# Performance work log

Measured on AMD Instinct MI355X. Metric: run time of the kernel, lower is better.

The kernel has to match this reference:

```python
import jax, jax.numpy as jnp
import numpy as np

L, H, M, KB = 8, 512, 32, 256  # layers, hidden, fourier modes, key bits
EPS = 1e-5


def setup_inputs() -> dict:
    key = jax.random.key(0)
    ks = jax.random.split(key, 20)
    B, S = 8, 2048
    s = 0.02
    return {
        'x': jax.random.normal(ks[0], (B, S), jnp.float32),
        # input projection Linear(1, H): weight [H] (squeezed), bias [H]
        'in_w': jax.random.normal(ks[1], (H,), jnp.float32) * s,
        'in_b': jax.random.normal(ks[2], (H,), jnp.float32) * s,
        # per-layer fourier weights (complex, stored as real/imag), conv1d(k=1), layernorm
        'fw_r': jax.random.normal(ks[3], (L, M, H, H), jnp.float32) * s,
        'fw_i': jax.random.normal(ks[4], (L, M, H, H), jnp.float32) * s,
        'conv_w': jax.random.normal(ks[5], (L, H, H), jnp.float32) / np.sqrt(H),
        'conv_b': jax.random.normal(ks[6], (L, H), jnp.float32) * s,
        'ln_g': jnp.ones((L, H), jnp.float32),
        'ln_b': jnp.zeros((L, H), jnp.float32),
        # output projection H -> H/2 -> H/4 -> 1
        'op1_w': jax.random.normal(ks[7], (H // 2, H), jnp.float32) / np.sqrt(H),
        'op1_b': jnp.zeros((H // 2,), jnp.float32),
        'op2_w': jax.random.normal(ks[8], (H // 4, H // 2), jnp.float32) / np.sqrt(H // 2),
        'op2_b': jnp.zeros((H // 4,), jnp.float32),
        'op3_w': jax.random.normal(ks[9], (1, H // 4), jnp.float32) / np.sqrt(H // 4),
        'op3_b': jnp.zeros((1,), jnp.float32),
        # cryptanalytic head H -> H -> KB (sigmoid)
        'h1_w': jax.random.normal(ks[10], (H, H), jnp.float32) / np.sqrt(H),
        'h1_b': jnp.zeros((H,), jnp.float32),
        'h2_w': jax.random.normal(ks[11], (KB, H), jnp.float32) / np.sqrt(H),
        'h2_b': jnp.zeros((KB,), jnp.float32),
    }


def _gelu(x):
    return jax.nn.gelu(x, approximate=False)


def _fourier_layer(x, Wc, cw, cb, g, b):
    # x: [B, S, H]; Wc: [M, H, H] complex
    S = x.shape[1]
    x_ft = jnp.fft.rfft(x, axis=1)  # [B, F, H] complex, F = S//2+1
    m = min(M, x_ft.shape[1])
    # batched per-mode complex GEMM (replaces python loop over modes)
    spec = jnp.einsum('bmh,mhk->bmk', x_ft[:, :m], Wc[:m])
    out_ft = jnp.concatenate([spec, jnp.zeros_like(x_ft[:, m:])], axis=1)
    x_fourier = jnp.fft.irfft(out_ft, n=S, axis=1)  # real [B, S, H]
    x_conv = x @ cw.T + cb  # Conv1d kernel-size-1 == per-position linear
    y = x_fourier + x_conv
    mu = jnp.mean(y, axis=-1, keepdims=True)
    var = jnp.var(y, axis=-1, keepdims=True)
    return (y - mu) * jax.lax.rsqrt(var + EPS) * g + b


def reference(x, in_w, in_b, fw_r, fw_i, conv_w, conv_b, ln_g, ln_b,
              op1_w, op1_b, op2_w, op2_b, op3_w, op3_b,
              h1_w, h1_b, h2_w, h2_b):
    # input projection: Linear(1, H) on x[..., None]
    h = x[:, :, None] * in_w[None, None, :] + in_b  # [B, S, H]
    Wc = fw_r + 1j * fw_i  # [L, M, H, H]
    for l in range(L):
        h = _fourier_layer(h, Wc[l], conv_w[l], conv_b[l], ln_g[l], ln_b[l]) + h
    # output projection (dropout is identity in eval)
    o = _gelu(h @ op1_w.T + op1_b)
    o = _gelu(o @ op2_w.T + op2_b)
    output = (o @ op3_w.T + op3_b)[..., 0]  # [B, S]
    gf = jnp.mean(h, axis=1)  # [B, H]
    k = _gelu(gf @ h1_w.T + h1_b)
    key_pred = jax.nn.sigmoid(k @ h2_w.T + h2_b)  # [B, KB]
    return output, key_pred
```

## Files before the change

kernel.cpp:

```cpp
#include <hip/hip_runtime.h>
#include <hip/hip_bf16.h>
#include <math.h>

#define BB   8
#define SEQ  2048
#define HD   512
#define LAY  8
#define MD   32
#define NKB  256
#define LNEPS 1e-5f

typedef __attribute__((ext_vector_type(8))) short v8s;
typedef __attribute__((ext_vector_type(4))) float v4f;
typedef __attribute__((ext_vector_type(4))) unsigned short v4us;

__device__ __forceinline__ float b2f(__hip_bfloat16 v) { return __bfloat162float(v); }
__device__ __forceinline__ float geluf(float v) { return v * 0.5f * (1.f + erff(v * 0.70710678118654752f)); }

__device__ __forceinline__ float ldin(const void* p, size_t i, int bf) {
    if (bf) return __bfloat162float(((const __hip_bfloat16*)p)[i]);
    return ((const float*)p)[i];
}
__device__ __forceinline__ void stout(void* p, size_t i, float v, int bf) {
    if (bf) ((__hip_bfloat16*)p)[i] = __float2bfloat16(v);
    else    ((float*)p)[i] = v;
}

__device__ __forceinline__ void gl2lds16(const void* g, void* l) {
    __builtin_amdgcn_global_load_lds((__attribute__((address_space(1))) void*)g,
                                     (__attribute__((address_space(3))) void*)l, 16, 0, 0);
}

__global__ void k_flag(const unsigned int* __restrict__ lng_bits, int* __restrict__ flag) {
    if (threadIdx.x == 0 && blockIdx.x == 0)
        *flag = (lng_bits[0] == 0x3F803F80u) ? 1 : 0;
}

__global__ void k_ffwd(__hip_bfloat16* __restrict__ F) {
    int idx = blockIdx.x * 256 + threadIdx.x;
    int j = idx >> 11, s = idx & 2047;
    int m = j >> 1;
    int phase = (m * s) & (SEQ - 1);
    float ang = (float)phase * (6.283185307179586f / (float)SEQ);
    float v = (j & 1) ? -sinf(ang) : cosf(ang);
    F[idx] = __float2bfloat16(v);
}

__global__ void k_t2(__hip_bfloat16* __restrict__ T2) {
    int idx = blockIdx.x * 256 + threadIdx.x;
    int s = idx >> 6, j = idx & 63;
    int m = j >> 1;
    float v;
    if (j == 0)      v = 1.f / (float)SEQ;
    else if (j == 1) v = 0.f;
    else {
        int phase = (m * s) & (SEQ - 1);
        float ang = (float)phase * (6.283185307179586f / (float)SEQ);
        v = (j & 1) ? (-2.f / (float)SEQ) * sinf(ang) : (2.f / (float)SEQ) * cosf(ang);
    }
    T2[idx] = __float2bfloat16(v);
}

__global__ void k_cwbf(const void* __restrict__ cw, __hip_bfloat16* __restrict__ dst,
                       const int* __restrict__ flag) {
    int bf = *flag;
    int idx = blockIdx.x * 256 + threadIdx.x;
    dst[idx] = __float2bfloat16(ldin(cw, idx, bf));
}

__global__ void k_bfcvt(const void* __restrict__ src, __hip_bfloat16* __restrict__ dst,
                        int n, const int* __restrict__ flag) {
    int bf = *flag;
    int idx = blockIdx.x * 256 + threadIdx.x;
    if (idx < n) dst[idx] = __float2bfloat16(ldin(src, idx, bf));
}

__global__ void k_tr(const void* __restrict__ src, float* __restrict__ dst, int log2R, int C, int n,
                     const int* __restrict__ flag) {
    int bf = *flag;
    int idx = blockIdx.x * 256 + threadIdx.x;
    if (idx >= n) return;
    int R = 1 << log2R;
    int r = idx & (R - 1);
    int c = idx >> log2R;
    dst[idx] = ldin(src, (size_t)r * C + c, bf);
}

__global__ void k_in(const void* __restrict__ x, const void* __restrict__ in_w, const void* __restrict__ in_b,
                     float* __restrict__ h, __hip_bfloat16* __restrict__ hbf, const int* __restrict__ flag) {
    int bf = *flag;
    int idx = blockIdx.x * 256 + threadIdx.x;
    int j = idx & 511;
    int bs = idx >> 9;
    float v = ldin(x, bs, bf) * ldin(in_w, j, bf) + ldin(in_b, j, bf);
    h[idx] = v;
    hbf[idx] = __float2bfloat16(v);
}

__global__ __launch_bounds__(256) void k_fdft2(const __hip_bfloat16* __restrict__ hbf,
                                               const __hip_bfloat16* __restrict__ Ffwd,
                                               float* __restrict__ Xft) {
    __shared__ __align__(16) __hip_bfloat16 Als[16 * 72];
    int t = threadIdx.x;
    int lane = t & 63, wv = t >> 6;
    int ln15 = lane & 15, quad = lane >> 4;
    int ht = blockIdx.x, b = blockIdx.y;
    int sr = t >> 2, hc = (t & 3) * 4;

    v4f acc = (v4f){0.f, 0.f, 0.f, 0.f};

    const __hip_bfloat16* asrc0 = hbf + (size_t)b * SEQ * HD + ht * 16;
    const __hip_bfloat16* fbase = Ffwd + (size_t)(wv * 16 + ln15) * SEQ + quad * 8;

    v4us cur = *(const v4us*)(asrc0 + (size_t)sr * HD + hc);
    for (int kc = 0; kc < 32; kc++) {
#pragma unroll
        for (int e = 0; e < 4; e++)
            Als[(hc + e) * 72 + sr] = ((const __hip_bfloat16*)&cur)[e];
        __syncthreads();
        v4us nxt = cur;
        if (kc < 31)
            nxt = *(const v4us*)(asrc0 + (size_t)((kc + 1) * 64 + sr) * HD + hc);
        v8s bf0 = *(const v8s*)(fbase + kc * 64);
        v8s bf1 = *(const v8s*)(fbase + kc * 64 + 32);
        v8s af0 = *(const v8s*)&Als[ln15 * 72 + quad * 8];
        v8s af1 = *(const v8s*)&Als[ln15 * 72 + 32 + quad * 8];
        acc = __builtin_amdgcn_mfma_f32_16x16x32_bf16(af0, bf0, acc, 0, 0, 0);
        acc = __builtin_amdgcn_mfma_f32_16x16x32_bf16(af1, bf1, acc, 0, 0, 0);
        __syncthreads();
        cur = nxt;
    }
    int j = wv * 16 + ln15;
    int m = j >> 1, c = j & 1;
    int hg = ht * 16 + quad * 4;
#pragma unroll
    for (int r = 0; r < 4; r++)
        Xft[(size_t)(b * 32 + m) * 1024 + (size_t)(hg + r) * 2 + c] = acc[r];
}

__global__ __launch_bounds__(512) void k_mix(const float* __restrict__ Xft,
                                             const void* __restrict__ fwr, const void* __restrict__ fwi,
                                             __hip_bfloat16* __restrict__ spec2, int l,
                                             const int* __restrict__ flag) {
    int bf = *flag;
    int kt = blockIdx.x;
    int m  = blockIdx.y;
    int t = threadIdx.x;
    int kl = t & 31, hg = t >> 5;
    int k0 = kt * 64 + kl * 2;
    __shared__ float xs[8192];
    __shared__ float red[16 * 512];
    for (int e = t; e < 8192; e += 512) {
        int b = e >> 10, r = e & 1023;
        xs[b * 1024 + r] = Xft[(size_t)(b * 32 + m) * 1024 + r];
    }
    __syncthreads();
    float ar0[8], ar1[8], ai0[8], ai1[8];
#pragma unroll
    for (int b = 0; b < 8; b++) { ar0[b] = 0.f; ar1[b] = 0.f; ai0[b] = 0.f; ai1[b] = 0.f; }
    size_t wbase = (size_t)(l * 32 + m) * 262144 + k0;
    const float2* xs2 = (const float2*)xs;
    if (bf) {
        const __hip_bfloat16* fr = (const __hip_bfloat16*)fwr;
        const __hip_bfloat16* fi = (const __hip_bfloat16*)fwi;
        for (int hh = hg; hh < 512; hh += 16) {
            unsigned int ur = *(const unsigned int*)(fr + wbase + (size_t)hh * 512);
            unsigned int ui = *(const unsigned int*)(fi + wbase + (size_t)hh * 512);
            float wr0 = __uint_as_float((ur & 0xFFFFu) << 16);
            float wr1 = __uint_as_float(ur & 0xFFFF0000u);
            float wi0 = __uint_as_float((ui & 0xFFFFu) << 16);
            float wi1 = __uint_as_float(ui & 0xFFFF0000u);
#pragma unroll
            for (int b = 0; b < 8; b++) {
                float2 x2 = xs2[b * 512 + hh];
                ar0[b] += x2.x * wr0 - x2.y * wi0;  ai0[b] += x2.x * wi0 + x2.y * wr0;
                ar1[b] += x2.x * wr1 - x2.y * wi1;  ai1[b] += x2.x * wi1 + x2.y * wr1;
            }
        }
    } else {
        const float* fr = (const float*)fwr;
        const float* fi = (const float*)fwi;
        for (int hh = hg; hh < 512; hh += 16) {
            float2 fr2 = *(const float2*)(fr + wbase + (size_t)hh * 512);
            float2 fi2 = *(const float2*)(fi + wbase + (size_t)hh * 512);
#pragma unroll
            for (int b = 0; b < 8; b++) {
                float2 x2 = xs2[b * 512 + hh];
                ar0[b] += x2.x * fr2.x - x2.y * fi2.x;  ai0[b] += x2.x * fi2.x + x2.y * fr2.x;
                ar1[b] += x2.x * fr2.y - x2.y * fi2.y;  ai1[b] += x2.x * fi2.y + x2.y * fr2.y;
            }
        }
    }
#pragma unroll
    for (int b = 0; b < 8; b++) {
        red[hg * 512 + b * 64 + kl * 2]     = ar0[b];
        red[hg * 512 + b * 64 + kl * 2 + 1] = ar1[b];
    }
    __syncthreads();
    float sr = 0.f;
#pragma unroll
    for (int g = 0; g < 16; g++) sr += red[g * 512 + t];
    __syncthreads();
#pragma unroll
    for (int b = 0; b < 8; b++) {
        red[hg * 512 + b * 64 + kl * 2]     = ai0[b];
        red[hg * 512 + b * 64 + kl * 2 + 1] = ai1[b];
    }
    __syncthreads();
    float si = 0.f;
#pragma unroll
    for (int g = 0; g < 16; g++) si += red[g * 512 + t];

    int b = t >> 6, j = t & 63;
    int k = kt * 64 + j;
    size_t o = ((size_t)(b * 512 + k) << 6) + 2 * m;
    __hip_bfloat16 hr = __float2bfloat16(sr), hi = __float2bfloat16(si);
    unsigned int pk = (unsigned int)*(unsigned short*)&hr | ((unsigned int)*(unsigned short*)&hi << 16);
    *(unsigned int*)(spec2 + o) = pk;
}

__global__ __launch_bounds__(256) void k_gemm(const __hip_bfloat16* __restrict__ hbf,
                                              const __hip_bfloat16* __restrict__ cwbf,
                                              const __hip_bfloat16* __restrict__ T2,
                                              const __hip_bfloat16* __restrict__ spec2,
                                              const void* __restrict__ cb,
                                              __hip_bfloat16* __restrict__ ybf,
                                              int l, const int* __restrict__ flag) {
    int bfv = *flag;
    __shared__ __hip_bfloat16 Als[128 * 32];
    __shared__ __hip_bfloat16 Bls[128 * 32];
    int t = threadIdx.x;
    int lane = t & 63, wv = t >> 6;
    int wr = wv >> 1, wc = wv & 1;
    int ln15 = lane & 15, quad = lane >> 4;
    int row0 = blockIdx.x * 128, n0 = blockIdx.y * 128;
    int b = row0 >> 11;
    int s0 = row0 & 2047;

    v4f acc[16];
#pragma unroll
    for (int i = 0; i < 16; i++) acc[i] = (v4f){0.f, 0.f, 0.f, 0.f};

    const __hip_bfloat16* cwl = cwbf + (size_t)l * 262144;
    for (int kc = 0; kc < 18; kc++) {
        int k0 = kc * 32;
#pragma unroll
        for (int p = 0; p < 2; p++) {
            int i = p * 256 + t;
            int row = i >> 2, kq = (i & 3) * 8;
            const __hip_bfloat16 *asrc, *bsrc;
            if (k0 < 512) {
                asrc = hbf + (size_t)(row0 + row) * 512 + k0 + kq;
                bsrc = cwl + (size_t)(n0 + row) * 512 + k0 + kq;
            } else {
                asrc = T2 + (size_t)(s0 + row) * 64 + (k0 - 512) + kq;
                bsrc = spec2 + (size_t)(b * 512 + n0 + row) * 64 + (k0 - 512) + kq;
            }
            gl2lds16(asrc, &Als[(size_t)(p * 256 + wv * 64) * 8]);
            gl2lds16(bsrc, &Bls[(size_t)(p * 256 + wv * 64) * 8]);
        }
        __syncthreads();
        v8s af[4], bfr[4];
#pragma unroll
        for (int i = 0; i < 4; i++)
            af[i] = *(const v8s*)&Als[(wr * 64 + i * 16 + ln15) * 32 + quad * 8];
#pragma unroll
        for (int j = 0; j < 4; j++)
            bfr[j] = *(const v8s*)&Bls[(wc * 64 + j * 16 + ln15) * 32 + quad * 8];
#pragma unroll
        for (int i = 0; i < 4; i++)
#pragma unroll
            for (int j = 0; j < 4; j++)
                acc[i * 4 + j] = __builtin_amdgcn_mfma_f32_16x16x32_bf16(af[i], bfr[j], acc[i * 4 + j], 0, 0, 0);
        __syncthreads();
    }
#pragma unroll
    for (int j = 0; j < 4; j++) {
        int col = n0 + wc * 64 + j * 16 + ln15;
        float cbv = ldin(cb, l * HD + col, bfv);
#pragma unroll
        for (int i = 0; i < 4; i++) {
            int rg = row0 + wr * 64 + i * 16 + quad * 4;
#pragma unroll
            for (int r = 0; r < 4; r++)
                ybf[(size_t)(rg + r) * HD + col] = __float2bfloat16(acc[i * 4 + j][r] + cbv);
        }
    }
}

__global__ __launch_bounds__(256) void k_ln(const __hip_bfloat16* __restrict__ ybf,
                                            const void* __restrict__ g, const void* __restrict__ bb,
                                            float* __restrict__ h, __hip_bfloat16* __restrict__ hbf,
                                            int l, const int* __restrict__ flag) {
    int bf = *flag;
    int row = blockIdx.x;
    int t = threadIdx.x;
    const unsigned int* yr = (const unsigned int*)(ybf + (size_t)row * HD);
    unsigned int u = yr[t];
    float v0 = __uint_as_float((u & 0xFFFFu) << 16);
    float v1 = __uint_as_float(u & 0xFFFF0000u);
    float s = v0 + v1, q = v0 * v0 + v1 * v1;
#pragma unroll
    for (int o = 32; o > 0; o >>= 1) { s += __shfl_down(s, o); q += __shfl_down(q, o); }
    __shared__ float sm[8];
    __shared__ float mv[2];
    int wid = t >> 6;
    if ((t & 63) == 0) { sm[wid] = s; sm[wid + 4] = q; }
    __syncthreads();
    if (t == 0) {
        float S = sm[0] + sm[1] + sm[2] + sm[3];
        float Q = sm[4] + sm[5] + sm[6] + sm[7];
        float mu = S * (1.f / (float)HD);
        float var = Q * (1.f / (float)HD) - mu * mu;
        mv[0] = mu; mv[1] = rsqrtf(var + LNEPS);
    }
    __syncthreads();
    float mu = mv[0], rs = mv[1];
    float2* hr2 = (float2*)(h + (size_t)row * HD);
    float2 hv = hr2[t];
    float n0 = (v0 - mu) * rs * ldin(g, l * HD + 2 * t, bf)     + ldin(bb, l * HD + 2 * t, bf)     + hv.x;
    float n1 = (v1 - mu) * rs * ldin(g, l * HD + 2 * t + 1, bf) + ldin(bb, l * HD + 2 * t + 1, bf) + hv.y;
    hr2[t] = (float2){n0, n1};
    __hip_bfloat16 a0 = __float2bfloat16(n0), a1 = __float2bfloat16(n1);
    unsigned int up = ((unsigned int)(*(unsigned short*)&a1) << 16) | (unsigned int)(*(unsigned short*)&a0);
    ((unsigned int*)(hbf + (size_t)row * HD))[t] = up;
}

__global__ __launch_bounds__(256) void k_pj1(const __hip_bfloat16* __restrict__ hbf,
                                             const __hip_bfloat16* __restrict__ w1bf,
                                             const void* __restrict__ b1,
                                             __hip_bfloat16* __restrict__ o1bf,
                                             const int* __restrict__ flag) {
    int bfv = *flag;
    __shared__ __hip_bfloat16 Als[128 * 32];
    __shared__ __hip_bfloat16 Bls[128 * 32];
    int t = threadIdx.x;
    int lane = t & 63, wv = t >> 6;
    int wr = wv >> 1, wc = wv & 1;
    int ln15 = lane & 15, quad = lane >> 4;
    int row0 = blockIdx.x * 128, n0 = blockIdx.y * 128;

    v4f acc[16];
#pragma unroll
    for (int i = 0; i < 16; i++) acc[i] = (v4f){0.f, 0.f, 0.f, 0.f};

    for (int kc = 0; kc < 16; kc++) {
        int k0 = kc * 32;
#pragma unroll
        for (int p = 0; p < 2; p++) {
            int i = p * 256 + t;
            int row = i >> 2, kq = (i & 3) * 8;
            gl2lds16(hbf + (size_t)(row0 + row) * 512 + k0 + kq, &Als[(size_t)(p * 256 + wv * 64) * 8]);
            gl2lds16(w1bf + (size_t)(n0 + row) * 512 + k0 + kq, &Bls[(size_t)(p * 256 + wv * 64) * 8]);
        }
        __syncthreads();
        v8s af[4], bfr[4];
#pragma unroll
        for (int i = 0; i < 4; i++)
            af[i] = *(const v8s*)&Als[(wr * 64 + i * 16 + ln15) * 32 + quad * 8];
#pragma unroll
        for (int j = 0; j < 4; j++)
            bfr[j] = *(const v8s*)&Bls[(wc * 64 + j * 16 + ln15) * 32 + quad * 8];
#pragma unroll
        for (int i = 0; i < 4; i++)
#pragma unroll
            for (int j = 0; j < 4; j++)
                acc[i * 4 + j] = __builtin_amdgcn_mfma_f32_16x16x32_bf16(af[i], bfr[j], acc[i * 4 + j], 0, 0, 0);
        __syncthreads();
    }
#pragma unroll
    for (int j = 0; j < 4; j++) {
        int col = n0 + wc * 64 + j * 16 + ln15;
        float bv = ldin(b1, col, bfv);
#pragma unroll
        for (int i = 0; i < 4; i++) {
            int rg = row0 + wr * 64 + i * 16 + quad * 4;
#pragma unroll
            for (int r = 0; r < 4; r++)
                o1bf[(size_t)(rg + r) * 256 + col] = __float2bfloat16(geluf(acc[i * 4 + j][r] + bv));
        }
    }
}

__global__ __launch_bounds__(256) void k_pj2(const __hip_bfloat16* __restrict__ o1bf,
                                             const __hip_bfloat16* __restrict__ w2bf,
                                             const void* __restrict__ b2,
                                             const void* __restrict__ w3, const void* __restrict__ b3,
                                             void* __restrict__ out, const int* __restrict__ flag) {
    int bfv = *flag;
    __shared__ __hip_bfloat16 Als[128 * 32];
    __shared__ __hip_bfloat16 Bls[128 * 32];
    __shared__ __hip_bfloat16 o2s[128 * 130];
    __shared__ float w3s[128];
    int t = threadIdx.x;
    int lane = t & 63, wv = t >> 6;
    int wr = wv >> 1, wc = wv & 1;
    int ln15 = lane & 15, quad = lane >> 4;
    int row0 = blockIdx.x * 128;
    if (t < 128) w3s[t] = ldin(w3, t, bfv);

    v4f acc[16];
#pragma unroll
    for (int i = 0; i < 16; i++) acc[i] = (v4f){0.f, 0.f, 0.f, 0.f};

    for (int kc = 0; kc < 8; kc++) {
        int k0 = kc * 32;
#pragma unroll
        for (int p = 0; p < 2; p++) {
            int i = p * 256 + t;
            int row = i >> 2, kq = (i & 3) * 8;
            gl2lds16(o1bf + (size_t)(row0 + row) * 256 + k0 + kq, &Als[(size_t)(p * 256 + wv * 64) * 8]);
            gl2lds16(w2bf + (size_t)row * 256 + k0 + kq,          &Bls[(size_t)(p * 256 + wv * 64) * 8]);
        }
        __syncthreads();
        v8s af[4], bfr[4];
#pragma unroll
        for (int i = 0; i < 4; i++)
            af[i] = *(const v8s*)&Als[(wr * 64 + i * 16 + ln15) * 32 + quad * 8];
#pragma unroll
        for (int j = 0; j < 4; j++)
            bfr[j] = *(const v8s*)&Bls[(wc * 64 + j * 16 + ln15) * 32 + quad * 8];
#pragma unroll
        for (int i = 0; i < 4; i++)
#pragma unroll
            for (int j = 0; j < 4; j++)
                acc[i * 4 + j] = __builtin_amdgcn_mfma_f32_16x16x32_bf16(af[i], bfr[j], acc[i * 4 + j], 0, 0, 0);
        __syncthreads();
    }
#pragma unroll
    for (int j = 0; j < 4; j++) {
        int col = wc * 64 + j * 16 + ln15;
        float bv = ldin(b2, col, bfv);
#pragma unroll
        for (int i = 0; i < 4; i++) {
            int rl = wr * 64 + i * 16 + quad * 4;
#pragma unroll
            for (int r = 0; r < 4; r++)
                o2s[(rl + r) * 130 + col] = __float2bfloat16(geluf(acc[i * 4 + j][r] + bv));
        }
    }
    __syncthreads();
    if (t < 128) {
        float s = 0.f;
        for (int j = 0; j < 128; j++) s += b2f(o2s[t * 130 + j]) * w3s[j];
        stout(out, row0 + t, s + ldin(b3, 0, bfv), bfv);
    }
}

__global__ void k_zero(float* p, int n) {
    int i = blockIdx.x * 256 + threadIdx.x;
    if (i < n) p[i] = 0.f;
}

__global__ __launch_bounds__(512) void k_gf(const float* __restrict__ h, float* __restrict__ gf) {
    int sc = blockIdx.x, b = blockIdx.y;
    int j = threadIdx.x;
    const float* p = h + ((size_t)b * SEQ + sc * 64) * HD + j;
    float s = 0.f;
    for (int i = 0; i < 64; i++) s += p[(size_t)i * HD];
    atomicAdd(&gf[b * HD + j], s * (1.f / (float)SEQ));
}

__global__ __launch_bounds__(512) void k_head(const float* __restrict__ gf,
                                              const float* __restrict__ h1T, const void* __restrict__ h1b,
                                              const float* __restrict__ h2T, const void* __restrict__ h2b,
                                              void* __restrict__ out, const int* __restrict__ flag) {
    int bf = *flag;
    int b = blockIdx.x;
    int t = threadIdx.x;
    __shared__ float gs[512];
    __shared__ float ks[512];
    gs[t] = gf[b * HD + t];
    __syncthreads();
    float a = 0.f;
    for (int j = 0; j < 512; j++) a += gs[j] * h1T[j * 512 + t];
    ks[t] = geluf(a + ldin(h1b, t, bf));
    __syncthreads();
    if (t < 256) {
        float s = 0.f;
        for (int j = 0; j < 512; j++) s += ks[j] * h2T[j * 256 + t];
        s += ldin(h2b, t, bf);
        stout(out, BB * SEQ + b * NKB + t, 1.f / (1.f + expf(-s)), bf);
    }
}

extern "C" void kernel_launch(void* const* d_in, const int* in_sizes, int n_in,
                              void* d_out, int out_size, void* d_ws, size_t ws_size,
                              hipStream_t stream) {
    const void* x    = d_in[0];
    const void* in_w = d_in[1];
    const void* in_b = d_in[2];
    const void* fwr  = d_in[3];
    const void* fwi  = d_in[4];
    const void* cw   = d_in[5];
    const void* cb   = d_in[6];
    const void* lng  = d_in[7];
    const void* lnb  = d_in[8];
    const void* w1   = d_in[9];
    const void* b1   = d_in[10];
    const void* w2   = d_in[11];
    const void* b2   = d_in[12];
    const void* w3   = d_in[13];
    const void* b3   = d_in[14];
    const void* h1w  = d_in[15];
    const void* h1b  = d_in[16];
    const void* h2w  = d_in[17];
    const void* h2b  = d_in[18];

    float* ws = (float*)d_ws;
    __hip_bfloat16* Ffwd = (__hip_bfloat16*)ws;
    float*          h    = ws + 131072;
    float*          Xp   = h + 8388608;
    __hip_bfloat16* ybf  = (__hip_bfloat16*)Xp;
    __hip_bfloat16* hbf  = (__hip_bfloat16*)(Xp + 4194304);
    __hip_bfloat16* cwbf = (__hip_bfloat16*)(Xp + 8388608);
    __hip_bfloat16* T2   = (__hip_bfloat16*)(Xp + 10485760);
    __hip_bfloat16* spec2= (__hip_bfloat16*)(Xp + 10551296);
    float*          Xft  = Xp + 10682368;
    float*          gf   = Xft + 262144;
    float*          w1T  = gf + 4096;
    __hip_bfloat16* w1bf = (__hip_bfloat16*)w1T;
    __hip_bfloat16* w2bf = (__hip_bfloat16*)(w1T + 65536);
    float*          w2T  = w1T + 131072;
    float*          h1T  = w2T + 32768;
    float*          h2T  = h1T + 262144;
    int*            flag = (int*)(h2T + 131072);
    __hip_bfloat16* o1bf = ybf;

    k_flag<<<1, 1, 0, stream>>>((const unsigned int*)lng, flag);
    k_ffwd<<<512, 256, 0, stream>>>(Ffwd);
    k_t2<<<512, 256, 0, stream>>>(T2);
    k_cwbf<<<8192, 256, 0, stream>>>(cw, cwbf, flag);
    k_bfcvt<<<512, 256, 0, stream>>>(w1, w1bf, 131072, flag);
    k_bfcvt<<<128, 256, 0, stream>>>(w2, w2bf, 32768, flag);
    k_tr<<<1024, 256, 0, stream>>>(h1w, h1T, 9, 512, 262144, flag);
    k_tr<<<512, 256, 0, stream>>>(h2w, h2T, 8, 512, 131072, flag);
    k_in<<<32768, 256, 0, stream>>>(x, in_w, in_b, h, hbf, flag);

    for (int l = 0; l < LAY; l++) {
        k_fdft2<<<dim3(32, 8), 256, 0, stream>>>(hbf, Ffwd, Xft);
        k_mix<<<dim3(8, 32), 512, 0, stream>>>(Xft, fwr, fwi, spec2, l, flag);
        k_gemm<<<dim3(128, 4), 256, 0, stream>>>(hbf, cwbf, T2, spec2, cb, ybf, l, flag);
        k_ln<<<16384, 256, 0, stream>>>(ybf, lng, lnb, h, hbf, l, flag);
    }

    k_zero<<<16, 256, 0, stream>>>(gf, 4096);
    k_gf<<<dim3(32, 8), 512, 0, stream>>>(h, gf);
    k_pj1<<<dim3(128, 2), 256, 0, stream>>>(hbf, w1bf, b1, o1bf, flag);
    k_pj2<<<128, 256, 0, stream>>>(o1bf, w2bf, b2, w3, b3, d_out, flag);
    k_head<<<8, 512, 0, stream>>>(gf, h1T, h1b, h2T, h2b, d_out, flag);
}
```

Baseline: 1.260 ms.

## Fuse GEMM with LayerNorm, split-K the forward DFT, merge setup kernels

Eight setup kernels plus the Xft and gf zeroing are merged into one block-dispatched k_setup kernel. The conv GEMM and LayerNorm are fused into k_gln: each block computes a full 64x512 output row tile and normalises it in LDS, so the bf16 ybf round trip to global memory and one launch per layer are gone. k_gln also zeroes Xft for the next layer. k_fdft2 is split along K across two blocks with an LDS double buffer and accumulates into Xft with atomicAdd. k_mix now handles four output columns per thread with vector weight loads. The costs are float atomics, which make the sum order nondeterministic, and fewer, larger blocks in the fused GEMM, which lowers parallelism.

```diff
diff --git a/kernel.cpp b/kernel.cpp
--- a/kernel.cpp
+++ b/kernel.cpp
@@ -16,6 +16,8 @@
 
 __device__ __forceinline__ float b2f(__hip_bfloat16 v) { return __bfloat162float(v); }
 __device__ __forceinline__ float geluf(float v) { return v * 0.5f * (1.f + erff(v * 0.70710678118654752f)); }
+__device__ __forceinline__ float bflo(unsigned int u) { return __uint_as_float((u & 0xFFFFu) << 16); }
+__device__ __forceinline__ float bfhi(unsigned int u) { return __uint_as_float(u & 0xFFFF0000u); }
 
 __device__ __forceinline__ float ldin(const void* p, size_t i, int bf) {
     if (bf) return __bfloat162float(((const __hip_bfloat16*)p)[i]);
@@ -36,75 +38,79 @@
         *flag = (lng_bits[0] == 0x3F803F80u) ? 1 : 0;
 }
 
-__global__ void k_ffwd(__hip_bfloat16* __restrict__ F) {
-    int idx = blockIdx.x * 256 + threadIdx.x;
-    int j = idx >> 11, s = idx & 2047;
-    int m = j >> 1;
-    int phase = (m * s) & (SEQ - 1);
-    float ang = (float)phase * (6.283185307179586f / (float)SEQ);
-    float v = (j & 1) ? -sinf(ang) : cosf(ang);
-    F[idx] = __float2bfloat16(v);
-}
-
-__global__ void k_t2(__hip_bfloat16* __restrict__ T2) {
-    int idx = blockIdx.x * 256 + threadIdx.x;
-    int s = idx >> 6, j = idx & 63;
-    int m = j >> 1;
-    float v;
-    if (j == 0)      v = 1.f / (float)SEQ;
-    else if (j == 1) v = 0.f;
-    else {
+__global__ void k_setup(const void* __restrict__ x, const void* __restrict__ in_w, const void* __restrict__ in_b,
+                        const void* __restrict__ cw, const void* __restrict__ w1, const void* __restrict__ w2,
+                        const void* __restrict__ h1w, const void* __restrict__ h2w,
+                        __hip_bfloat16* __restrict__ Ffwd, __hip_bfloat16* __restrict__ T2,
+                        __hip_bfloat16* __restrict__ cwbf, __hip_bfloat16* __restrict__ w1bf,
+                        __hip_bfloat16* __restrict__ w2bf, float* __restrict__ h1T, float* __restrict__ h2T,
+                        float* __restrict__ h, __hip_bfloat16* __restrict__ hbf,
+                        float* __restrict__ Xft, float* __restrict__ gf,
+                        const int* __restrict__ flag) {
+    int bf = *flag;
+    int blk = blockIdx.x, t = threadIdx.x;
+    if (blk < 512) {
+        int idx = blk * 256 + t;
+        int j = idx >> 11, s = idx & 2047;
+        int m = j >> 1;
         int phase = (m * s) & (SEQ - 1);
         float ang = (float)phase * (6.283185307179586f / (float)SEQ);
-        v = (j & 1) ? (-2.f / (float)SEQ) * sinf(ang) : (2.f / (float)SEQ) * cosf(ang);
-    }
-    T2[idx] = __float2bfloat16(v);
-}
-
-__global__ void k_cwbf(const void* __restrict__ cw, __hip_bfloat16* __restrict__ dst,
-                       const int* __restrict__ flag) {
-    int bf = *flag;
-    int idx = blockIdx.x * 256 + threadIdx.x;
-    dst[idx] = __float2bfloat16(ldin(cw, idx, bf));
-}
-
-__global__ void k_bfcvt(const void* __restrict__ src, __hip_bfloat16* __restrict__ dst,
-                        int n, const int* __restrict__ flag) {
-    int bf = *flag;
-    int idx = blockIdx.x * 256 + threadIdx.x;
-    if (idx < n) dst[idx] = __float2bfloat16(ldin(src, idx, bf));
-}
-
-__global__ void k_tr(const void* __restrict__ src, float* __restrict__ dst, int log2R, int C, int n,
-                     const int* __restrict__ flag) {
-    int bf = *flag;
-    int idx = blockIdx.x * 256 + threadIdx.x;
-    if (idx >= n) return;
-    int R = 1 << log2R;
-    int r = idx & (R - 1);
-    int c = idx >> log2R;
-    dst[idx] = ldin(src, (size_t)r * C + c, bf);
-}
-
-__global__ void k_in(const void* __restrict__ x, const void* __restrict__ in_w, const void* __restrict__ in_b,
-                     float* __restrict__ h, __hip_bfloat16* __restrict__ hbf, const int* __restrict__ flag) {
-    int bf = *flag;
-    int idx = blockIdx.x * 256 + threadIdx.x;
-    int j = idx & 511;
-    int bs = idx >> 9;
-    float v = ldin(x, bs, bf) * ldin(in_w, j, bf) + ldin(in_b, j, bf);
-    h[idx] = v;
-    hbf[idx] = __float2bfloat16(v);
+        Ffwd[idx] = __float2bfloat16((j & 1) ? -sinf(ang) : cosf(ang));
+    } else if (blk < 1024) {
+        int idx = (blk - 512) * 256 + t;
+        int s = idx >> 6, j = idx & 63;
+        int m = j >> 1;
+        float v;
+        if (j == 0)      v = 1.f / (float)SEQ;
+        else if (j == 1) v = 0.f;
+        else {
+            int phase = (m * s) & (SEQ - 1);
+            float ang = (float)phase * (6.283185307179586f / (float)SEQ);
+            v = (j & 1) ? (-2.f / (float)SEQ) * sinf(ang) : (2.f / (float)SEQ) * cosf(ang);
+        }
+        T2[idx] = __float2bfloat16(v);
+    } else if (blk < 9216) {
+        int idx = (blk - 1024) * 256 + t;
+        cwbf[idx] = __float2bfloat16(ldin(cw, idx, bf));
+    } else if (blk < 9728) {
+        int idx = (blk - 9216) * 256 + t;
+        w1bf[idx] = __float2bfloat16(ldin(w1, idx, bf));
+    } else if (blk < 9856) {
+        int idx = (blk - 9728) * 256 + t;
+        w2bf[idx] = __float2bfloat16(ldin(w2, idx, bf));
+    } else if (blk < 10880) {
+        int idx = (blk - 9856) * 256 + t;
+        int r = idx & 511, c = idx >> 9;
+        h1T[idx] = ldin(h1w, (size_t)r * 512 + c, bf);
+    } else if (blk < 11392) {
+        int idx = (blk - 10880) * 256 + t;
+        int r = idx & 255, c = idx >> 8;
+        h2T[idx] = ldin(h2w, (size_t)r * 512 + c, bf);
+    } else if (blk < 12416) {
+        int idx = (blk - 11392) * 256 + t;
+        Xft[idx] = 0.f;
+    } else if (blk < 12432) {
+        int idx = (blk - 12416) * 256 + t;
+        gf[idx] = 0.f;
+    } else {
+        int idx = (blk - 12432) * 256 + t;
+        int j = idx & 511;
+        int bs = idx >> 9;
+        float v = ldin(x, bs, bf) * ldin(in_w, j, bf) + ldin(in_b, j, bf);
+        h[idx] = v;
+        hbf[idx] = __float2bfloat16(v);
+    }
 }
 
 __global__ __launch_bounds__(256) void k_fdft2(const __hip_bfloat16* __restrict__ hbf,
                                                const __hip_bfloat16* __restrict__ Ffwd,
                                                float* __restrict__ Xft) {
-    __shared__ __align__(16) __hip_bfloat16 Als[16 * 72];
+    __shared__ __align__(16) __hip_bfloat16 Als[2][16 * 72];
     int t = threadIdx.x;
     int lane = t & 63, wv = t >> 6;
     int ln15 = lane & 15, quad = lane >> 4;
-    int ht = blockIdx.x, b = blockIdx.y;
+    int ht = blockIdx.x, b = blockIdx.y, kh = blockIdx.z;
+    int kcs = kh * 16;
     int sr = t >> 2, hc = (t & 3) * 4;
 
     v4f acc = (v4f){0.f, 0.f, 0.f, 0.f};
@@ -112,21 +118,27 @@
     const __hip_bfloat16* asrc0 = hbf + (size_t)b * SEQ * HD + ht * 16;
     const __hip_bfloat16* fbase = Ffwd + (size_t)(wv * 16 + ln15) * SEQ + quad * 8;
 
-    v4us cur = *(const v4us*)(asrc0 + (size_t)sr * HD + hc);
-    for (int kc = 0; kc < 32; kc++) {
-#pragma unroll
-        for (int e = 0; e < 4; e++)
-            Als[(hc + e) * 72 + sr] = ((const __hip_bfloat16*)&cur)[e];
-        __syncthreads();
+    v4us cur = *(const v4us*)(asrc0 + (size_t)(kcs * 64 + sr) * HD + hc);
+#pragma unroll
+    for (int e = 0; e < 4; e++)
+        Als[0][(hc + e) * 72 + sr] = ((const __hip_bfloat16*)&cur)[e];
+    __syncthreads();
+    for (int i = 0; i < 16; i++) {
+        int buf = i & 1;
         v4us nxt = cur;
-        if (kc < 31)
-            nxt = *(const v4us*)(asrc0 + (size_t)((kc + 1) * 64 + sr) * HD + hc);
-        v8s bf0 = *(const v8s*)(fbase + kc * 64);
-        v8s bf1 = *(const v8s*)(fbase + kc * 64 + 32);
-        v8s af0 = *(const v8s*)&Als[ln15 * 72 + quad * 8];
-        v8s af1 = *(const v8s*)&Als[ln15 * 72 + 32 + quad * 8];
+        if (i < 15)
+            nxt = *(const v4us*)(asrc0 + (size_t)((kcs + i + 1) * 64 + sr) * HD + hc);
+        v8s bf0 = *(const v8s*)(fbase + (kcs + i) * 64);
+        v8s bf1 = *(const v8s*)(fbase + (kcs + i) * 64 + 32);
+        v8s af0 = *(const v8s*)&Als[buf][ln15 * 72 + quad * 8];
+        v8s af1 = *(const v8s*)&Als[buf][ln15 * 72 + 32 + quad * 8];
         acc = __builtin_amdgcn_mfma_f32_16x16x32_bf16(af0, bf0, acc, 0, 0, 0);
         acc = __builtin_amdgcn_mfma_f32_16x16x32_bf16(af1, bf1, acc, 0, 0, 0);
+        if (i < 15) {
+#pragma unroll
+            for (int e = 0; e < 4; e++)
+                Als[buf ^ 1][(hc + e) * 72 + sr] = ((const __hip_bfloat16*)&nxt)[e];
+        }
         __syncthreads();
         cur = nxt;
     }
@@ -135,7 +147,7 @@
     int hg = ht * 16 + quad * 4;
 #pragma unroll
     for (int r = 0; r < 4; r++)
-        Xft[(size_t)(b * 32 + m) * 1024 + (size_t)(hg + r) * 2 + c] = acc[r];
+        atomicAdd(&Xft[(size_t)(b * 32 + m) * 1024 + (size_t)(hg + r) * 2 + c], acc[r]);
 }
 
 __global__ __launch_bounds__(512) void k_mix(const float* __restrict__ Xft,
@@ -146,96 +158,113 @@
     int kt = blockIdx.x;
     int m  = blockIdx.y;
     int t = threadIdx.x;
-    int kl = t & 31, hg = t >> 5;
-    int k0 = kt * 64 + kl * 2;
+    int kl = t & 15, hg = t >> 4;
+    int k0 = kt * 64 + kl * 4;
     __shared__ float xs[8192];
-    __shared__ float red[16 * 512];
+    __shared__ float red[32 * 512];
     for (int e = t; e < 8192; e += 512) {
-        int b = e >> 10, r = e & 1023;
-        xs[b * 1024 + r] = Xft[(size_t)(b * 32 + m) * 1024 + r];
-    }
-    __syncthreads();
-    float ar0[8], ar1[8], ai0[8], ai1[8];
-#pragma unroll
-    for (int b = 0; b < 8; b++) { ar0[b] = 0.f; ar1[b] = 0.f; ai0[b] = 0.f; ai1[b] = 0.f; }
+        int bb = e >> 10, r = e & 1023;
+        xs[bb * 1024 + r] = Xft[(size_t)(bb * 32 + m) * 1024 + r];
+    }
+    __syncthreads();
+    float ar[8][4], ai[8][4];
+#pragma unroll
+    for (int bb = 0; bb < 8; bb++)
+#pragma unroll
+        for (int q = 0; q < 4; q++) { ar[bb][q] = 0.f; ai[bb][q] = 0.f; }
     size_t wbase = (size_t)(l * 32 + m) * 262144 + k0;
     const float2* xs2 = (const float2*)xs;
     if (bf) {
         const __hip_bfloat16* fr = (const __hip_bfloat16*)fwr;
         const __hip_bfloat16* fi = (const __hip_bfloat16*)fwi;
-        for (int hh = hg; hh < 512; hh += 16) {
-            unsigned int ur = *(const unsigned int*)(fr + wbase + (size_t)hh * 512);
-            unsigned int ui = *(const unsigned int*)(fi + wbase + (size_t)hh * 512);
-            float wr0 = __uint_as_float((ur & 0xFFFFu) << 16);
-            float wr1 = __uint_as_float(ur & 0xFFFF0000u);
-            float wi0 = __uint_as_float((ui & 0xFFFFu) << 16);
-            float wi1 = __uint_as_float(ui & 0xFFFF0000u);
-#pragma unroll
-            for (int b = 0; b < 8; b++) {
-                float2 x2 = xs2[b * 512 + hh];
-                ar0[b] += x2.x * wr0 - x2.y * wi0;  ai0[b] += x2.x * wi0 + x2.y * wr0;
-                ar1[b] += x2.x * wr1 - x2.y * wi1;  ai1[b] += x2.x * wi1 + x2.y * wr1;
+        for (int hh = hg; hh < 512; hh += 32) {
+            v4us urv = *(const v4us*)(fr + wbase + (size_t)hh * 512);
+            v4us uiv = *(const v4us*)(fi + wbase + (size_t)hh * 512);
+            float wr[4], wi[4];
+#pragma unroll
+            for (int q = 0; q < 4; q++) {
+                wr[q] = __uint_as_float(((unsigned int)(unsigned short)urv[q]) << 16);
+                wi[q] = __uint_as_float(((unsigned int)(unsigned short)uiv[q]) << 16);
+            }
+#pragma unroll
+            for (int bb = 0; bb < 8; bb++) {
+                float2 x2 = xs2[bb * 512 + hh];
+#pragma unroll
+                for (int q = 0; q < 4; q++) {
+                    ar[bb][q] += x2.x * wr[q] - x2.y * wi[q];
+                    ai[bb][q] += x2.x * wi[q] + x2.y * wr[q];
+                }
             }
         }
     } else {
         const float* fr = (const float*)fwr;
         const float* fi = (const float*)fwi;
-        for (int hh = hg; hh < 512; hh += 16) {
-            float2 fr2 = *(const float2*)(fr + wbase + (size_t)hh * 512);
-            float2 fi2 = *(const float2*)(fi + wbase + (size_t)hh * 512);
-#pragma unroll
-            for (int b = 0; b < 8; b++) {
-                float2 x2 = xs2[b * 512 + hh];
-                ar0[b] += x2.x * fr2.x - x2.y * fi2.x;  ai0[b] += x2.x * fi2.x + x2.y * fr2.x;
-                ar1[b] += x2.x * fr2.y - x2.y * fi2.y;  ai1[b] += x2.x * fi2.y + x2.y * fr2.y;
+        for (int hh = hg; hh < 512; hh += 32) {
+            v4f wrv = *(const v4f*)(fr + wbase + (size_t)hh * 512);
+            v4f wiv = *(const v4f*)(fi + wbase + (size_t)hh * 512);
+#pragma unroll
+            for (int bb = 0; bb < 8; bb++) {
+                float2 x2 = xs2[bb * 512 + hh];
+#pragma unroll
+                for (int q = 0; q < 4; q++) {
+                    ar[bb][q] += x2.x * wrv[q] - x2.y * wiv[q];
+                    ai[bb][q] += x2.x * wiv[q] + x2.y * wrv[q];
+                }
             }
         }
     }
-#pragma unroll
-    for (int b = 0; b < 8; b++) {
-        red[hg * 512 + b * 64 + kl * 2]     = ar0[b];
-        red[hg * 512 + b * 64 + kl * 2 + 1] = ar1[b];
-    }
+    v4f* red4 = (v4f*)red;
+#pragma unroll
+    for (int bb = 0; bb < 8; bb++)
+        red4[hg * 128 + bb * 16 + kl] = (v4f){ar[bb][0], ar[bb][1], ar[bb][2], ar[bb][3]};
     __syncthreads();
     float sr = 0.f;
 #pragma unroll
-    for (int g = 0; g < 16; g++) sr += red[g * 512 + t];
-    __syncthreads();
-#pragma unroll
-    for (int b = 0; b < 8; b++) {
-        red[hg * 512 + b * 64 + kl * 2]     = ai0[b];
-        red[hg * 512 + b * 64 + kl * 2 + 1] = ai1[b];
-    }
+    for (int g = 0; g < 32; g++) sr += red[g * 512 + t];
+    __syncthreads();
+#pragma unroll
+    for (int bb = 0; bb < 8; bb++)
+        red4[hg * 128 + bb * 16 + kl] = (v4f){ai[bb][0], ai[bb][1], ai[bb][2], ai[bb][3]};
     __syncthreads();
     float si = 0.f;
 #pragma unroll
-    for (int g = 0; g < 16; g++) si += red[g * 512 + t];
-
-    int b = t >> 6, j = t & 63;
+    for (int g = 0; g < 32; g++) si += red[g * 512 + t];
+
+    int bb = t >> 6, j = t & 63;
     int k = kt * 64 + j;
-    size_t o = ((size_t)(b * 512 + k) << 6) + 2 * m;
+    size_t o = ((size_t)(bb * 512 + k) << 6) + 2 * m;
     __hip_bfloat16 hr = __float2bfloat16(sr), hi = __float2bfloat16(si);
     unsigned int pk = (unsigned int)*(unsigned short*)&hr | ((unsigned int)*(unsigned short*)&hi << 16);
     *(unsigned int*)(spec2 + o) = pk;
 }
 
-__global__ __launch_bounds__(256) void k_gemm(const __hip_bfloat16* __restrict__ hbf,
-                                              const __hip_bfloat16* __restrict__ cwbf,
-                                              const __hip_bfloat16* __restrict__ T2,
-                                              const __hip_bfloat16* __restrict__ spec2,
-                                              const void* __restrict__ cb,
-                                              __hip_bfloat16* __restrict__ ybf,
-                                              int l, const int* __restrict__ flag) {
+__global__ __launch_bounds__(512) void k_gln(__hip_bfloat16* __restrict__ hbf,
+                                             const __hip_bfloat16* __restrict__ cwbf,
+                                             const __hip_bfloat16* __restrict__ T2,
+                                             const __hip_bfloat16* __restrict__ spec2,
+                                             const void* __restrict__ cb,
+                                             const void* __restrict__ lng, const void* __restrict__ lnb,
+                                             float* __restrict__ h,
+                                             float* __restrict__ Xft,
+                                             int l, const int* __restrict__ flag) {
     int bfv = *flag;
-    __shared__ __hip_bfloat16 Als[128 * 32];
-    __shared__ __hip_bfloat16 Bls[128 * 32];
+    __shared__ __align__(16) __hip_bfloat16 smem[64 * 520];
+    __shared__ float stats[128];
+    __hip_bfloat16* Als = smem;
+    __hip_bfloat16* Bls = smem + 2048;
+    __hip_bfloat16* Yls = smem;
+
     int t = threadIdx.x;
     int lane = t & 63, wv = t >> 6;
-    int wr = wv >> 1, wc = wv & 1;
+    int wr = wv >> 2, wc = wv & 3;
     int ln15 = lane & 15, quad = lane >> 4;
-    int row0 = blockIdx.x * 128, n0 = blockIdx.y * 128;
-    int b = row0 >> 11;
-    int s0 = row0 & 2047;
+    int row0 = blockIdx.x * 64;
+    int b = row0 >> 11, s0 = row0 & 2047;
+
+    {
+        float* xz = Xft + (size_t)blockIdx.x * 1024;
+        xz[t] = 0.f; xz[t + 512] = 0.f;
+    }
 
     v4f acc[16];
 #pragma unroll
@@ -244,86 +273,85 @@
     const __hip_bfloat16* cwl = cwbf + (size_t)l * 262144;
     for (int kc = 0; kc < 18; kc++) {
         int k0 = kc * 32;
-#pragma unroll
-        for (int p = 0; p < 2; p++) {
-            int i = p * 256 + t;
-            int row = i >> 2, kq = (i & 3) * 8;
-            const __hip_bfloat16 *asrc, *bsrc;
-            if (k0 < 512) {
-                asrc = hbf + (size_t)(row0 + row) * 512 + k0 + kq;
-                bsrc = cwl + (size_t)(n0 + row) * 512 + k0 + kq;
-            } else {
-                asrc = T2 + (size_t)(s0 + row) * 64 + (k0 - 512) + kq;
-                bsrc = spec2 + (size_t)(b * 512 + n0 + row) * 64 + (k0 - 512) + kq;
-            }
-            gl2lds16(asrc, &Als[(size_t)(p * 256 + wv * 64) * 8]);
-            gl2lds16(bsrc, &Bls[(size_t)(p * 256 + wv * 64) * 8]);
-        }
-        __syncthreads();
-        v8s af[4], bfr[4];
-#pragma unroll
-        for (int i = 0; i < 4; i++)
-            af[i] = *(const v8s*)&Als[(wr * 64 + i * 16 + ln15) * 32 + quad * 8];
-#pragma unroll
-        for (int j = 0; j < 4; j++)
-            bfr[j] = *(const v8s*)&Bls[(wc * 64 + j * 16 + ln15) * 32 + quad * 8];
-#pragma unroll
-        for (int i = 0; i < 4; i++)
-#pragma unroll
-            for (int j = 0; j < 4; j++)
-                acc[i * 4 + j] = __builtin_amdgcn_mfma_f32_16x16x32_bf16(af[i], bfr[j], acc[i * 4 + j], 0, 0, 0);
-        __syncthreads();
-    }
-#pragma unroll
-    for (int j = 0; j < 4; j++) {
-        int col = n0 + wc * 64 + j * 16 + ln15;
+        if (t < 256) {
+            int row = t >> 2, kq = (t & 3) * 8;
+            const __hip_bfloat16* asrc = (k0 < 512)
+                ? hbf + (size_t)(row0 + row) * 512 + k0 + kq
+                : T2 + (size_t)(s0 + row) * 64 + (k0 - 512) + kq;
+            gl2lds16(asrc, &Als[(size_t)(wv * 64) * 8]);
+        }
+#pragma unroll
+        for (int p = 0; p < 4; p++) {
+            int i = p * 512 + t;
+            int n = i >> 2, kq = (i & 3) * 8;
+            const __hip_bfloat16* bsrc = (k0 < 512)
+                ? cwl + (size_t)n * 512 + k0 + kq
+                : spec2 + (size_t)(b * 512 + n) * 64 + (k0 - 512) + kq;
+            gl2lds16(bsrc, &Bls[(size_t)(p * 512 + wv * 64) * 8]);
+        }
+        __syncthreads();
+        v8s af[2], bfr[8];
+#pragma unroll
+        for (int i = 0; i < 2; i++)
+            af[i] = *(const v8s*)&Als[(wr * 32 + i * 16 + ln15) * 32 + quad * 8];
+#pragma unroll
+        for (int j = 0; j < 8; j++)
+            bfr[j] = *(const v8s*)&Bls[(wc * 128 + j * 16 + ln15) * 32 + quad * 8];
+#pragma unroll
+        for (int i = 0; i < 2; i++)
+#pragma unroll
+            for (int j = 0; j < 8; j++)
+                acc[i * 8 + j] = __builtin_amdgcn_mfma_f32_16x16x32_bf16(af[i], bfr[j], acc[i * 8 + j], 0, 0, 0);
+        __syncthreads();
+    }
+#pragma unroll
+    for (int j = 0; j < 8; j++) {
+        int col = wc * 128 + j * 16 + ln15;
         float cbv = ldin(cb, l * HD + col, bfv);
 #pragma unroll
-        for (int i = 0; i < 4; i++) {
-            int rg = row0 + wr * 64 + i * 16 + quad * 4;
+        for (int i = 0; i < 2; i++) {
+            int rl = wr * 32 + i * 16 + quad * 4;
 #pragma unroll
             for (int r = 0; r < 4; r++)
-                ybf[(size_t)(rg + r) * HD + col] = __float2bfloat16(acc[i * 4 + j][r] + cbv);
-        }
-    }
-}
-
-__global__ __launch_bounds__(256) void k_ln(const __hip_bfloat16* __restrict__ ybf,
-                                            const void* __restrict__ g, const void* __restrict__ bb,
-                                            float* __restrict__ h, __hip_bfloat16* __restrict__ hbf,
-                                            int l, const int* __restrict__ flag) {
-    int bf = *flag;
-    int row = blockIdx.x;
-    int t = threadIdx.x;
-    const unsigned int* yr = (const unsigned int*)(ybf + (size_t)row * HD);
-    unsigned int u = yr[t];
-    float v0 = __uint_as_float((u & 0xFFFFu) << 16);
-    float v1 = __uint_as_float(u & 0xFFFF0000u);
-    float s = v0 + v1, q = v0 * v0 + v1 * v1;
-#pragma unroll
-    for (int o = 32; o > 0; o >>= 1) { s += __shfl_down(s, o); q += __shfl_down(q, o); }
-    __shared__ float sm[8];
-    __shared__ float mv[2];
-    int wid = t >> 6;
-    if ((t & 63) == 0) { sm[wid] = s; sm[wid + 4] = q; }
-    __syncthreads();
-    if (t == 0) {
-        float S = sm[0] + sm[1] + sm[2] + sm[3];
-        float Q = sm[4] + sm[5] + sm[6] + sm[7];
-        float mu = S * (1.f / (float)HD);
-        float var = Q * (1.f / (float)HD) - mu * mu;
-        mv[0] = mu; mv[1] = rsqrtf(var + LNEPS);
-    }
-    __syncthreads();
-    float mu = mv[0], rs = mv[1];
-    float2* hr2 = (float2*)(h + (size_t)row * HD);
-    float2 hv = hr2[t];
-    float n0 = (v0 - mu) * rs * ldin(g, l * HD + 2 * t, bf)     + ldin(bb, l * HD + 2 * t, bf)     + hv.x;
-    float n1 = (v1 - mu) * rs * ldin(g, l * HD + 2 * t + 1, bf) + ldin(bb, l * HD + 2 * t + 1, bf) + hv.y;
-    hr2[t] = (float2){n0, n1};
-    __hip_bfloat16 a0 = __float2bfloat16(n0), a1 = __float2bfloat16(n1);
-    unsigned int up = ((unsigned int)(*(unsigned short*)&a1) << 16) | (unsigned int)(*(unsigned short*)&a0);
-    ((unsigned int*)(hbf + (size_t)row * HD))[t] = up;
+                Yls[(rl + r) * 520 + col] = __float2bfloat16(acc[i * 8 + j][r] + cbv);
+        }
+    }
+    __syncthreads();
+    {
+        int r = t >> 3, g = t & 7;
+        float s = 0.f, q = 0.f;
+        for (int i = 0; i < 32; i++) {
+            int cp = g + i * 8;
+            unsigned int u = *(const unsigned int*)&Yls[r * 520 + cp * 2];
+            float v0 = bflo(u), v1 = bfhi(u);
+            s += v0 + v1; q += v0 * v0 + v1 * v1;
+        }
+        s += __shfl_xor(s, 1); s += __shfl_xor(s, 2); s += __shfl_xor(s, 4);
+        q += __shfl_xor(q, 1); q += __shfl_xor(q, 2); q += __shfl_xor(q, 4);
+        if (g == 0) {
+            float mu = s * (1.f / (float)HD);
+            float var = q * (1.f / (float)HD) - mu * mu;
+            stats[r * 2] = mu; stats[r * 2 + 1] = rsqrtf(var + LNEPS);
+        }
+    }
+    __syncthreads();
+    for (int k = 0; k < 32; k++) {
+        int e2 = t + 512 * k;
+        int r = e2 >> 8, c2 = e2 & 255;
+        float mu = stats[r * 2], rs = stats[r * 2 + 1];
+        unsigned int u = *(const unsigned int*)&Yls[r * 520 + c2 * 2];
+        float v0 = bflo(u), v1 = bfhi(u);
+        int gc = 2 * c2;
+        float g0 = ldin(lng, l * HD + gc, bfv),     g1 = ldin(lng, l * HD + gc + 1, bfv);
+        float b0 = ldin(lnb, l * HD + gc, bfv),     b1 = ldin(lnb, l * HD + gc + 1, bfv);
+        float2 hv = *(const float2*)&h[(size_t)(row0 + r) * HD + gc];
+        float n0 = (v0 - mu) * rs * g0 + b0 + hv.x;
+        float n1 = (v1 - mu) * rs * g1 + b1 + hv.y;
+        *(float2*)&h[(size_t)(row0 + r) * HD + gc] = (float2){n0, n1};
+        __hip_bfloat16 a0 = __float2bfloat16(n0), a1 = __float2bfloat16(n1);
+        unsigned int up = ((unsigned int)(*(unsigned short*)&a1) << 16) | (unsigned int)(*(unsigned short*)&a0);
+        ((unsigned int*)(hbf + (size_t)(row0 + r) * HD))[c2] = up;
+    }
 }
 
 __global__ __launch_bounds__(256) void k_pj1(const __hip_bfloat16* __restrict__ hbf,
@@ -445,11 +473,6 @@
         for (int j = 0; j < 128; j++) s += b2f(o2s[t * 130 + j]) * w3s[j];
         stout(out, row0 + t, s + ldin(b3, 0, bfv), bfv);
     }
-}
-
-__global__ void k_zero(float* p, int n) {
-    int i = blockIdx.x * 256 + threadIdx.x;
-    if (i < n) p[i] = 0.f;
 }
 
 __global__ __launch_bounds__(512) void k_gf(const float* __restrict__ h, float* __restrict__ gf) {
@@ -511,7 +534,7 @@
     __hip_bfloat16* Ffwd = (__hip_bfloat16*)ws;
     float*          h    = ws + 131072;
     float*          Xp   = h + 8388608;
-    __hip_bfloat16* ybf  = (__hip_bfloat16*)Xp;
+    __hip_bfloat16* o1bf = (__hip_bfloat16*)Xp;
     __hip_bfloat16* hbf  = (__hip_bfloat16*)(Xp + 4194304);
     __hip_bfloat16* cwbf = (__hip_bfloat16*)(Xp + 8388608);
     __hip_bfloat16* T2   = (__hip_bfloat16*)(Xp + 10485760);
@@ -525,26 +548,18 @@
     float*          h1T  = w2T + 32768;
     float*          h2T  = h1T + 262144;
     int*            flag = (int*)(h2T + 131072);
-    __hip_bfloat16* o1bf = ybf;
 
     k_flag<<<1, 1, 0, stream>>>((const unsigned int*)lng, flag);
-    k_ffwd<<<512, 256, 0, stream>>>(Ffwd);
-    k_t2<<<512, 256, 0, stream>>>(T2);
-    k_cwbf<<<8192, 256, 0, stream>>>(cw, cwbf, flag);
-    k_bfcvt<<<512, 256, 0, stream>>>(w1, w1bf, 131072, flag);
-    k_bfcvt<<<128, 256, 0, stream>>>(w2, w2bf, 32768, flag);
-    k_tr<<<1024, 256, 0, stream>>>(h1w, h1T, 9, 512, 262144, flag);
-    k_tr<<<512, 256, 0, stream>>>(h2w, h2T, 8, 512, 131072, flag);
-    k_in<<<32768, 256, 0, stream>>>(x, in_w, in_b, h, hbf, flag);
+    k_setup<<<45200, 256, 0, stream>>>(x, in_w, in_b, cw, w1, w2, h1w, h2w,
+                                       Ffwd, T2, cwbf, w1bf, w2bf, h1T, h2T,
+                                       h, hbf, Xft, gf, flag);
 
     for (int l = 0; l < LAY; l++) {
-        k_fdft2<<<dim3(32, 8), 256, 0, stream>>>(hbf, Ffwd, Xft);
+        k_fdft2<<<dim3(32, 8, 2), 256, 0, stream>>>(hbf, Ffwd, Xft);
         k_mix<<<dim3(8, 32), 512, 0, stream>>>(Xft, fwr, fwi, spec2, l, flag);
-        k_gemm<<<dim3(128, 4), 256, 0, stream>>>(hbf, cwbf, T2, spec2, cb, ybf, l, flag);
-        k_ln<<<16384, 256, 0, stream>>>(ybf, lng, lnb, h, hbf, l, flag);
-    }
-
-    k_zero<<<16, 256, 0, stream>>>(gf, 4096);
+        k_gln<<<256, 512, 0, stream>>>(hbf, cwbf, T2, spec2, cb, lng, lnb, h, Xft, l, flag);
+    }
+
     k_gf<<<dim3(32, 8), 512, 0, stream>>>(h, gf);
     k_pj1<<<dim3(128, 2), 256, 0, stream>>>(hbf, w1bf, b1, o1bf, flag);
     k_pj2<<<128, 256, 0, stream>>>(o1bf, w2bf, b2, w3, b3, d_out, flag);
```

Measured after the change: 1.209 ms. -4.1%, faster.
